# Kernel tuning notes

Hardware: AMD Instinct MI355X
Metric: run time of the kernel (lower is better)

## Reference

```python
import jax, jax.numpy as jnp
import numpy as np

B, S, H, NH, NL = 8, 768, 768, 12, 5
HD = H // NH


def setup_inputs() -> dict:
    key = jax.random.key(0)
    ks = jax.random.split(key, 14)
    lim = 1.0 / np.sqrt(H)
    u = lambda k, shape: jax.random.uniform(k, shape, jnp.float32, -lim, lim)
    inp = {}
    inp["hidden_states"] = jax.random.normal(ks[0], (B, S, H), jnp.float32)
    inp["language_ids"] = jax.random.randint(ks[1], (B,), 0, NL)
    inp["attention_mask"] = jnp.ones((B, S), jnp.int32)
    # per-language query/key Linear weights (torch Linear: y = x @ W.T + b)
    inp["Wq_lang"] = u(ks[2], (NL, H, H))
    inp["bq_lang"] = u(ks[3], (NL, H))
    inp["Wk_lang"] = u(ks[4], (NL, H, H))
    inp["bk_lang"] = u(ks[5], (NL, H))
    # nn.MultiheadAttention params
    inp["in_proj_w"] = u(ks[6], (3 * H, H))
    inp["in_proj_b"] = u(ks[7], (3 * H,))
    inp["out_proj_w"] = u(ks[8], (H, H))
    inp["out_proj_b"] = u(ks[9], (H,))
    # alignment matrices: initialized as eye in torch; perturb so products are non-trivial
    inp["align"] = jnp.eye(H, dtype=jnp.float32) + 0.02 * jax.random.normal(ks[10], (NL, NL, H, H), jnp.float32)
    # output projection + layer norm
    inp["proj_w"] = u(ks[11], (H, H))
    inp["proj_b"] = u(ks[12], (H,))
    inp["ln_g"] = jnp.ones((H,), jnp.float32)
    inp["ln_b"] = jnp.zeros((H,), jnp.float32)
    return inp


def reference(hidden_states, language_ids, attention_mask, Wq_lang, bq_lang, Wk_lang, bk_lang,
              in_proj_w, in_proj_b, out_proj_w, out_proj_b, align, proj_w, proj_b, ln_g, ln_b):
    b, s, h = hidden_states.shape
    lang = language_ids
    # language-routed query/key transforms (grouped GEMM via gather of per-lang weights)
    q = jnp.einsum('bsi,boi->bso', hidden_states, Wq_lang[lang]) + bq_lang[lang][:, None, :]
    k = jnp.einsum('bsi,boi->bso', hidden_states, Wk_lang[lang]) + bk_lang[lang][:, None, :]
    # nn.MultiheadAttention (eval mode, no dropout). Note: the torch module's
    # key_padding_mask is always all-False due to a masked_fill(-inf).bool() bug,
    # so no masking is applied -- reproduced faithfully here.
    wq, wk, wv = jnp.split(in_proj_w, 3, axis=0)
    bq_, bk_, bv_ = jnp.split(in_proj_b, 3)
    Q = (jnp.einsum('bsi,oi->bso', q, wq) + bq_).reshape(b, s, NH, HD)
    K = (jnp.einsum('bsi,oi->bso', k, wk) + bk_).reshape(b, s, NH, HD)
    V = (jnp.einsum('bsi,oi->bso', hidden_states, wv) + bv_).reshape(b, s, NH, HD)
    scores = jnp.einsum('bqhd,bkhd->bhqk', Q, K) / np.sqrt(HD).astype(np.float32)
    attn = jax.nn.softmax(scores, axis=-1)  # [b, nh, s, s]
    ctx = jnp.einsum('bhqk,bkhd->bqhd', attn, V).reshape(b, s, h)
    aligned = jnp.einsum('bsi,oi->bso', ctx, out_proj_w) + out_proj_b
    # pairwise alignment chain: for each i, aligned_i @ prod_{j: lang_j != lang_i} A[lang_i, lang_j]
    # (i==j skipped; same-language pairs skipped since no A exists)
    same = lang[:, None] == lang[None, :]  # [b, b]; diagonal is True -> identity
    sel = align[lang[:, None], lang[None, :]]  # [b, b, h, h]
    I = jnp.eye(h, dtype=hidden_states.dtype)
    Smat = jnp.where(same[:, :, None, None], I, sel)  # [b(i), b(j), h, h]
    def step(carry, Sj):  # carry [b,h,h], Sj [b,h,h] for one j across all i
        return carry @ Sj, None
    M, _ = jax.lax.scan(step, jnp.tile(I, (b, 1, 1)), jnp.swapaxes(Smat, 0, 1))
    aligned = jnp.einsum('bsh,bhk->bsk', aligned, M)
    # output projection + residual layer norm
    out = jnp.einsum('bsi,oi->bso', aligned, proj_w) + proj_b
    x = out + hidden_states
    mu = x.mean(-1, keepdims=True)
    var = x.var(-1, keepdims=True)
    return (x - mu) / jnp.sqrt(var + 1e-5) * ln_g + ln_b
```

## Files before the change

kernel.cpp:

```cpp
#include <hip/hip_runtime.h>

#define Bn 8
#define Sn 768
#define Hn 768
#define NHn 12
#define HDn 64
#define NLn 5

typedef unsigned short u16;
typedef __bf16 bf16x8 __attribute__((ext_vector_type(8)));
typedef short s16x8 __attribute__((ext_vector_type(8)));
typedef float f32x4 __attribute__((ext_vector_type(4)));
typedef unsigned short u16x4 __attribute__((ext_vector_type(4)));

static __device__ __forceinline__ float bf2f(u16 v) {
    return __uint_as_float(((unsigned)v) << 16);
}
static __device__ __forceinline__ u16 f2bf(float f) {
    unsigned u = __float_as_uint(f);
    unsigned r = u + 0x7fffu + ((u >> 16) & 1u);
    return (u16)(r >> 16);
}
static __device__ __forceinline__ bf16x8 ld8(const u16* p) {
    return *reinterpret_cast<const bf16x8*>(p);
}
static __device__ __forceinline__ void glds16(const u16* g, u16* l) {
    __builtin_amdgcn_global_load_lds(
        (const __attribute__((address_space(1))) void*)g,
        (__attribute__((address_space(3))) void*)l, 16, 0, 0);
}

__global__ __launch_bounds__(256) void k_f2b3(
    const float* __restrict__ s0, u16* __restrict__ d0, int n0,
    const float* __restrict__ s1, u16* __restrict__ d1, int n1,
    const float* __restrict__ s2, u16* __restrict__ d2, int n2)
{
    int i = blockIdx.x * 256 + threadIdx.x;
    const float* s; u16* d; int off;
    if (i < n0)                { s = s0; d = d0; off = i; }
    else if (i < n0 + n1)      { s = s1; d = d1; off = i - n0; }
    else if (i < n0 + n1 + n2) { s = s2; d = d2; off = i - n0 - n1; }
    else return;
    float4 v = reinterpret_cast<const float4*>(s)[off];
    u16x4 o;
    o[0] = f2bf(v.x); o[1] = f2bf(v.y); o[2] = f2bf(v.z); o[3] = f2bf(v.w);
    reinterpret_cast<u16x4*>(d)[off] = o;
}

__global__ __launch_bounds__(256) void k_f2b1(
    const float* __restrict__ s, u16* __restrict__ d, int n)
{
    int i = blockIdx.x * 256 + threadIdx.x;
    if (i >= n) return;
    float4 v = reinterpret_cast<const float4*>(s)[i];
    u16x4 o;
    o[0] = f2bf(v.x); o[1] = f2bf(v.y); o[2] = f2bf(v.z); o[3] = f2bf(v.w);
    reinterpret_cast<u16x4*>(d)[i] = o;
}

__global__ __launch_bounds__(256) void k_transpose11(
    const float* __restrict__ Wq, const float* __restrict__ Wk,
    const float* __restrict__ opw, u16* __restrict__ S, u16* __restrict__ opwT)
{
    __shared__ float T[64][65];
    const size_t HH = (size_t)Hn * Hn;
    int z = blockIdx.z;
    const float* src;
    u16* dst;
    if (z < 5)       { src = Wq + (size_t)z * HH;       dst = S + (size_t)z * HH; }
    else if (z < 10) { src = Wk + (size_t)(z - 5) * HH; dst = S + (size_t)z * HH; }
    else             { src = opw;                        dst = opwT; }
    int i0 = blockIdx.x * 64, o0 = blockIdx.y * 64;
    int x = threadIdx.x & 63, ys = threadIdx.x >> 6;
    for (int r = ys; r < 64; r += 4)
        T[r][x] = src[(size_t)(o0 + r) * Hn + i0 + x];
    __syncthreads();
    for (int r = ys; r < 64; r += 4)
        dst[(size_t)(i0 + r) * Hn + o0 + x] = f2bf(T[x][r]);
}

__device__ __forceinline__ void gemm128(
    const u16* __restrict__ A, int lda,
    const u16* __restrict__ Bw, int ldb,
    const float* __restrict__ bias,
    const float* __restrict__ addres,
    u16* __restrict__ outH, float* __restrict__ outF,
    u16* __restrict__ outVT, int ldc,
    int K, int m0, int n0, float scale)
{
    __shared__ u16 As[2][128 * 32];
    __shared__ u16 Bs[2][128 * 32];
    const int tid = threadIdx.x;
    const int lane = tid & 63, wave = tid >> 6;
    const int lrow = lane & 15, lquad = lane >> 4;
    const int wm = (wave >> 1) * 64, wn = (wave & 1) * 64;

    const int s0 = tid, s1 = tid + 256;
    const u16* gA0 = A + (size_t)(m0 + (s0 >> 2)) * lda + (s0 & 3) * 8;
    const u16* gA1 = A + (size_t)(m0 + (s1 >> 2)) * lda + (s1 & 3) * 8;
    const u16* gB0 = Bw + (size_t)(n0 + (s0 >> 2)) * ldb + (s0 & 3) * 8;
    const u16* gB1 = Bw + (size_t)(n0 + (s1 >> 2)) * ldb + (s1 & 3) * 8;

    f32x4 z = {0.f, 0.f, 0.f, 0.f};
    f32x4 acc[4][4];
    #pragma unroll
    for (int i = 0; i < 4; ++i)
        #pragma unroll
        for (int j = 0; j < 4; ++j) acc[i][j] = z;

    const int NT = K >> 5;
    auto stage = [&](int buf, int k0) {
        glds16(gA0 + k0, &As[buf][s0 * 8]);
        glds16(gA1 + k0, &As[buf][s1 * 8]);
        glds16(gB0 + k0, &Bs[buf][s0 * 8]);
        glds16(gB1 + k0, &Bs[buf][s1 * 8]);
    };
    auto compute = [&](int buf) {
        bf16x8 af[4], bf_[4];
        #pragma unroll
        for (int i = 0; i < 4; ++i)
            af[i] = ld8(&As[buf][(wm + i * 16 + lrow) * 32 + lquad * 8]);
        #pragma unroll
        for (int j = 0; j < 4; ++j)
            bf_[j] = ld8(&Bs[buf][(wn + j * 16 + lrow) * 32 + lquad * 8]);
        #pragma unroll
        for (int i = 0; i < 4; ++i)
            #pragma unroll
            for (int j = 0; j < 4; ++j)
                acc[i][j] = __builtin_amdgcn_mfma_f32_16x16x32_bf16(af[i], bf_[j], acc[i][j], 0, 0, 0);
    };

    stage(0, 0);
    __syncthreads();
    for (int kt = 1; kt < NT; ++kt) {
        stage(kt & 1, kt * 32);
        compute((kt - 1) & 1);
        __syncthreads();
    }
    compute((NT - 1) & 1);

    #pragma unroll
    for (int i = 0; i < 4; ++i) {
        #pragma unroll
        for (int j = 0; j < 4; ++j) {
            int col = n0 + wn + j * 16 + lrow;
            float bv = bias ? bias[col] : 0.f;
            if (outVT) {
                int row0 = m0 + wm + i * 16 + lquad * 4;
                int bb = row0 / Sn, s = row0 % Sn;
                int hh = col >> 6, dd = col & 63;
                u16x4 o;
                #pragma unroll
                for (int r = 0; r < 4; ++r) o[r] = f2bf((acc[i][j][r] + bv) * scale);
                *reinterpret_cast<u16x4*>(
                    outVT + (((size_t)bb * NHn + hh) * 64 + dd) * Sn + s) = o;
            } else {
                #pragma unroll
                for (int r = 0; r < 4; ++r) {
                    int row = m0 + wm + i * 16 + lquad * 4 + r;
                    float v = (acc[i][j][r] + bv) * scale;
                    if (addres) v += addres[(size_t)row * ldc + col];
                    if (outF) outF[(size_t)row * ldc + col] = v;
                    else      outH[(size_t)row * ldc + col] = f2bf(v);
                }
            }
        }
    }
}

__device__ __forceinline__ void gemm64(
    const u16* __restrict__ A, const u16* __restrict__ Bw,
    u16* __restrict__ outH, int K, int m0, int n0)
{
    __shared__ u16 As[2][64 * 32];
    __shared__ u16 Bs[2][64 * 32];
    const int tid = threadIdx.x;
    const int lane = tid & 63, wave = tid >> 6;
    const int lrow = lane & 15, lquad = lane >> 4;
    const int wm = (wave >> 1) * 32, wn = (wave & 1) * 32;

    const int row = tid >> 2, seg = tid & 3;
    const u16* gA = A + (size_t)(m0 + row) * Hn + seg * 8;
    const u16* gB = Bw + (size_t)(n0 + row) * Hn + seg * 8;

    f32x4 z = {0.f, 0.f, 0.f, 0.f};
    f32x4 acc[2][2];
    #pragma unroll
    for (int i = 0; i < 2; ++i)
        #pragma unroll
        for (int j = 0; j < 2; ++j) acc[i][j] = z;

    const int NT = K >> 5;
    auto stage = [&](int buf, int k0) {
        glds16(gA + k0, &As[buf][tid * 8]);
        glds16(gB + k0, &Bs[buf][tid * 8]);
    };
    auto compute = [&](int buf) {
        bf16x8 af[2], bf_[2];
        #pragma unroll
        for (int i = 0; i < 2; ++i)
            af[i] = ld8(&As[buf][(wm + i * 16 + lrow) * 32 + lquad * 8]);
        #pragma unroll
        for (int j = 0; j < 2; ++j)
            bf_[j] = ld8(&Bs[buf][(wn + j * 16 + lrow) * 32 + lquad * 8]);
        #pragma unroll
        for (int i = 0; i < 2; ++i)
            #pragma unroll
            for (int j = 0; j < 2; ++j)
                acc[i][j] = __builtin_amdgcn_mfma_f32_16x16x32_bf16(af[i], bf_[j], acc[i][j], 0, 0, 0);
    };

    stage(0, 0);
    __syncthreads();
    for (int kt = 1; kt < NT; ++kt) {
        stage(kt & 1, kt * 32);
        compute((kt - 1) & 1);
        __syncthreads();
    }
    compute((NT - 1) & 1);

    #pragma unroll
    for (int i = 0; i < 2; ++i)
        #pragma unroll
        for (int j = 0; j < 2; ++j) {
            int col = n0 + wn + j * 16 + lrow;
            #pragma unroll
            for (int r = 0; r < 4; ++r) {
                int row_ = m0 + wm + i * 16 + lquad * 4 + r;
                outH[(size_t)row_ * Hn + col] = f2bf(acc[i][j][r]);
            }
        }
}


__global__ __launch_bounds__(256) void k_gemm_qkv(
    const u16* __restrict__ A,
    const u16* __restrict__ Sq, const u16* __restrict__ Sk,
    const u16* __restrict__ Wv,
    const float* __restrict__ beff, const float* __restrict__ ipb,
    const int* __restrict__ lang,
    u16* __restrict__ outQ, u16* __restrict__ outK, u16* __restrict__ outVT)
{
    const size_t HH = (size_t)Hn * Hn;
    int z = blockIdx.z;
    int m0 = blockIdx.x * 128, n0 = blockIdx.y * 128;
    int l = lang[blockIdx.x / 6];
    if (z == 0) {
        gemm128(A, Hn, Sq + (size_t)l * HH, Hn, beff + (size_t)l * Hn,
                nullptr, outQ, nullptr, nullptr, Hn, Hn, m0, n0, 0.125f);
    } else if (z == 1) {
        gemm128(A, Hn, Sk + (size_t)l * HH, Hn, beff + (size_t)(5 + l) * Hn,
                nullptr, outK, nullptr, nullptr, Hn, Hn, m0, n0, 1.f);
    } else {
        gemm128(A, Hn, Wv, Hn, ipb + 2 * Hn,
                nullptr, nullptr, nullptr, outVT, Hn, Hn, m0, n0, 1.f);
    }
}

__global__ __launch_bounds__(256) void k_gemm_act(
    const u16* __restrict__ A, const u16* __restrict__ W5,
    const float* __restrict__ bias5, const int* __restrict__ lang,
    u16* __restrict__ out, float scale)
{
    int b = blockIdx.x / 6;
    int l = lang ? lang[b] : 0;
    gemm128(A, Hn, W5 + (size_t)l * Hn * Hn, Hn,
            bias5 + (size_t)l * Hn, nullptr, out, nullptr, nullptr, Hn, Hn,
            blockIdx.x * 128, blockIdx.y * 128, scale);
}

__global__ __launch_bounds__(256) void k_comb10(
    const u16* __restrict__ ipwb, u16* __restrict__ S)
{
    const size_t HH = (size_t)Hn * Hn;
    int z = blockIdx.z;
    const u16* Aop = ipwb + (z < 5 ? 0 : HH);
    gemm128(Aop, Hn, S + (size_t)z * HH, Hn, nullptr, nullptr,
            S + (size_t)(10 + z) * HH, nullptr, nullptr, Hn, Hn,
            blockIdx.x * 128, blockIdx.y * 128, 1.f);
}

__global__ __launch_bounds__(256) void k_ybuild64(
    const u16* __restrict__ MT5, const u16* __restrict__ Bfix,
    u16* __restrict__ out5)
{
    size_t off = (size_t)blockIdx.z * Hn * Hn;
    gemm64(MT5 + off, Bfix, out5 + off, Hn,
           blockIdx.x * 64, blockIdx.y * 64);
}

__global__ __launch_bounds__(256) void k_xgemm(
    const u16* __restrict__ A, const u16* __restrict__ W,
    const float* __restrict__ bias, const float* __restrict__ hidden,
    float* __restrict__ x)
{
    gemm128(A, Hn, W, Hn, bias, hidden, nullptr, x, nullptr, Hn, Hn,
            blockIdx.x * 128, blockIdx.y * 128, 1.f);
}

__global__ __launch_bounds__(256) void k_chain_first(
    const u16* __restrict__ alignb, const int* __restrict__ lang,
    u16* __restrict__ out5)
{
    const size_t HH = (size_t)Hn * Hn;
    int l = blockIdx.z, lj = lang[Bn - 1];
    u16* dst = out5 + (size_t)l * HH;
    int i0 = blockIdx.x * 64, o0 = blockIdx.y * 64;
    const int tid = threadIdx.x;
    if (lj == l) {
        #pragma unroll
        for (int it = 0; it < 2; ++it) {
            int s = tid + 256 * it;
            int ri = s >> 3, c8 = s & 7;
            s16x8 v;
            #pragma unroll
            for (int e = 0; e < 8; ++e)
                v[e] = (short)((i0 + ri == o0 + c8 * 8 + e) ? 0x3F80 : 0);
            *reinterpret_cast<s16x8*>(dst + (size_t)(i0 + ri) * Hn + o0 + c8 * 8) = v;
        }
    } else {
        const u16* src = alignb + ((size_t)l * NLn + lj) * HH;
        __shared__ u16 T[64][72];
        #pragma unroll
        for (int it = 0; it < 2; ++it) {
            int s = tid + 256 * it;
            int r = s >> 3, c8 = s & 7;
            s16x8 v = *reinterpret_cast<const s16x8*>(
                src + (size_t)(o0 + r) * Hn + i0 + c8 * 8);
            #pragma unroll
            for (int e = 0; e < 8; ++e) T[c8 * 8 + e][r] = (u16)v[e];
        }
        __syncthreads();
        #pragma unroll
        for (int it = 0; it < 2; ++it) {
            int s = tid + 256 * it;
            int ri = s >> 3, c8 = s & 7;
            s16x8 v = *reinterpret_cast<const s16x8*>(&T[ri][c8 * 8]);
            *reinterpret_cast<s16x8*>(dst + (size_t)(i0 + ri) * Hn + o0 + c8 * 8) = v;
        }
    }
}

__global__ __launch_bounds__(256) void k_chain64(
    const u16* __restrict__ Pin, u16* __restrict__ Pout,
    const u16* __restrict__ alignb, const int* __restrict__ lang, int j)
{
    const size_t HH = (size_t)Hn * Hn;
    int l = blockIdx.z;
    int lj = lang[j];
    const u16* Pl = Pin + (size_t)l * HH;
    u16* Po = Pout + (size_t)l * HH;
    int m0 = blockIdx.x * 64, n0 = blockIdx.y * 64;
    if (lj == l) {
        int tid = threadIdx.x;
        #pragma unroll
        for (int it = 0; it < 2; ++it) {
            int s = tid + 256 * it;
            int row = s >> 3, seg = s & 7;
            *reinterpret_cast<s16x8*>(Po + (size_t)(m0 + row) * Hn + n0 + seg * 8) =
                *reinterpret_cast<const s16x8*>(Pl + (size_t)(m0 + row) * Hn + n0 + seg * 8);
        }
    } else {
        const u16* F = alignb + ((size_t)l * NLn + lj) * HH;
        gemm64(Pl, F, Po, Hn, m0, n0);
    }
}

__global__ __launch_bounds__(256) void k_biasqk(
    const float* __restrict__ ipw, const float* __restrict__ ipb,
    const float* __restrict__ bq_lang, const float* __restrict__ bk_lang,
    float* __restrict__ beff)
{
    int o = blockIdx.x * 256 + threadIdx.x;
    int which = blockIdx.y / 5, l = blockIdx.y % 5;
    const float4* w = reinterpret_cast<const float4*>(ipw + (size_t)which * Hn * Hn + (size_t)o * Hn);
    const float4* bv = reinterpret_cast<const float4*>(((which ? bk_lang : bq_lang) + (size_t)l * Hn));
    float s = 0.f;
    for (int j = 0; j < Hn / 4; ++j) {
        float4 a = w[j], b = bv[j];
        s += a.x * b.x + a.y * b.y + a.z * b.z + a.w * b.w;
    }
    s += ipb[which * Hn + o];
    beff[(size_t)(which * 5 + l) * Hn + o] = s;
}

__global__ __launch_bounds__(256) void k_opbeff(
    const float* __restrict__ opb, const u16* __restrict__ MT5,
    float* __restrict__ out)
{
    int n = blockIdx.x * 256 + threadIdx.x;
    int l = blockIdx.y;
    const u16* mt = MT5 + ((size_t)l * Hn + n) * Hn;
    float s = 0.f;
    for (int k = 0; k < Hn; k += 8) {
        s16x8 v = *reinterpret_cast<const s16x8*>(mt + k);
        #pragma unroll
        for (int j = 0; j < 8; ++j) s += opb[k + j] * bf2f((u16)v[j]);
    }
    out[(size_t)l * Hn + n] = s;
}

__global__ __launch_bounds__(256) void k_attn(
    const u16* __restrict__ Q, const u16* __restrict__ K,
    const u16* __restrict__ VT, u16* __restrict__ ctx)
{
    __shared__ u16 Ks[2][64 * 64];
    __shared__ u16 Vs[64 * 64];
    __shared__ u16 Pw[4][16 * 72];

    const int bz = blockIdx.z, h = blockIdx.y, q0 = blockIdx.x * 64;
    const int tid = threadIdx.x;
    const int wave = tid >> 6, lane = tid & 63;
    const int lrow = lane & 15, lquad = lane >> 4;
    const int sw = lrow & 7;

    const u16* Qp = Q + ((size_t)(bz * Sn + q0 + wave * 16 + lrow)) * Hn + h * HDn;
    const u16* Kb = K + (size_t)bz * Sn * Hn + h * HDn;
    const u16* Vb = VT + ((size_t)(bz * NHn + h) * 64) * Sn;

    bf16x8 qa0 = ld8(Qp + lquad * 8);
    bf16x8 qa1 = ld8(Qp + 32 + lquad * 8);

    f32x4 z4 = {0.f, 0.f, 0.f, 0.f};
    float m_r[4], l_l[4];
    f32x4 oacc[4];
    #pragma unroll
    for (int r = 0; r < 4; ++r) { m_r[r] = -1e30f; l_l[r] = 0.f; }
    #pragma unroll
    for (int jd = 0; jd < 4; ++jd) oacc[jd] = z4;

    const int vd0 = tid >> 3,        vp0 = (tid & 7) ^ (vd0 & 7);
    const int vd1 = (tid + 256) >> 3, vp1 = ((tid + 256) & 7) ^ (vd1 & 7);
    const u16* vg0 = Vb + (size_t)vd0 * Sn + vp0 * 8;
    const u16* vg1 = Vb + (size_t)vd1 * Sn + vp1 * 8;
    s16x8 vr0, vr1;

    auto vload = [&](int t0) {
        vr0 = *reinterpret_cast<const s16x8*>(vg0 + t0);
        vr1 = *reinterpret_cast<const s16x8*>(vg1 + t0);
    };
    auto vstore = [&]() {
        *reinterpret_cast<s16x8*>(&Vs[tid * 8]) = vr0;
        *reinterpret_cast<s16x8*>(&Vs[(tid + 256) * 8]) = vr1;
    };
    auto stageK = [&](int t0, int buf) {
        #pragma unroll
        for (int it = 0; it < 2; ++it) {
            int idx = tid + 256 * it;
            int row = idx >> 3, p = idx & 7;
            glds16(Kb + (size_t)(t0 + row) * Hn + (p ^ (row & 7)) * 8,
                   &Ks[buf][idx * 8]);
        }
    };

    auto compute = [&](int buf) {
        f32x4 sc[4];
        __builtin_amdgcn_s_setprio(1);
        #pragma unroll
        for (int j = 0; j < 4; ++j) {
            int base = (j * 16 + lrow) * 64 + ((lquad ^ sw) * 8);
            f32x4 s = __builtin_amdgcn_mfma_f32_16x16x32_bf16(qa0, ld8(&Ks[buf][base]), z4, 0, 0, 0);
            sc[j] = __builtin_amdgcn_mfma_f32_16x16x32_bf16(qa1, ld8(&Ks[buf][base ^ 32]), s, 0, 0, 0);
        }
        __builtin_amdgcn_s_setprio(0);
        float tmax[4];
        #pragma unroll
        for (int r = 0; r < 4; ++r)
            tmax[r] = fmaxf(fmaxf(sc[0][r], sc[1][r]), fmaxf(sc[2][r], sc[3][r]));
        #pragma unroll
        for (int off = 1; off < 16; off <<= 1)
            #pragma unroll
            for (int r = 0; r < 4; ++r)
                tmax[r] = fmaxf(tmax[r], __shfl_xor(tmax[r], off));
        bool grow = (tmax[0] > m_r[0]) | (tmax[1] > m_r[1]) |
                    (tmax[2] > m_r[2]) | (tmax[3] > m_r[3]);
        if (grow) {
            #pragma unroll
            for (int r = 0; r < 4; ++r) {
                float mn = fmaxf(m_r[r], tmax[r]);
                float a = __expf(m_r[r] - mn);
                m_r[r] = mn;
                l_l[r] *= a;
                #pragma unroll
                for (int jd = 0; jd < 4; ++jd) oacc[jd][r] *= a;
            }
        }
        float ps[4] = {0.f, 0.f, 0.f, 0.f};
        #pragma unroll
        for (int j = 0; j < 4; ++j)
            #pragma unroll
            for (int r = 0; r < 4; ++r) {
                float p = __expf(sc[j][r] - m_r[r]);
                ps[r] += p;
                Pw[wave][(lquad * 4 + r) * 72 + j * 16 + lrow] = f2bf(p);
            }
        #pragma unroll
        for (int r = 0; r < 4; ++r) l_l[r] += ps[r];
        bf16x8 pa0 = ld8(&Pw[wave][lrow * 72 + lquad * 8]);
        bf16x8 pa1 = ld8(&Pw[wave][lrow * 72 + 32 + lquad * 8]);
        __builtin_amdgcn_s_setprio(1);
        #pragma unroll
        for (int jd = 0; jd < 4; ++jd) {
            int vbase = (jd * 16 + lrow) * 64 + ((lquad ^ sw) * 8);
            oacc[jd] = __builtin_amdgcn_mfma_f32_16x16x32_bf16(pa0, ld8(&Vs[vbase]), oacc[jd], 0, 0, 0);
            oacc[jd] = __builtin_amdgcn_mfma_f32_16x16x32_bf16(pa1, ld8(&Vs[vbase ^ 32]), oacc[jd], 0, 0, 0);
        }
        __builtin_amdgcn_s_setprio(0);
    };

    stageK(0, 0);
    vload(0);
    vstore();
    __syncthreads();
    for (int kt = 0; kt < 12; ++kt) {
        if (kt < 11) {
            vload((kt + 1) * 64);
            stageK((kt + 1) * 64, (kt + 1) & 1);
        }
        compute(kt & 1);
        if (kt < 11) {
            __syncthreads();
            vstore();
            __syncthreads();
        }
    }

    #pragma unroll
    for (int off = 1; off < 16; off <<= 1)
        #pragma unroll
        for (int r = 0; r < 4; ++r)
            l_l[r] += __shfl_xor(l_l[r], off);

    float rl[4];
    #pragma unroll
    for (int r = 0; r < 4; ++r) rl[r] = 1.f / l_l[r];
    #pragma unroll
    for (int jd = 0; jd < 4; ++jd)
        #pragma unroll
        for (int r = 0; r < 4; ++r) {
            size_t row = (size_t)bz * Sn + q0 + wave * 16 + lquad * 4 + r;
            ctx[row * Hn + h * HDn + jd * 16 + lrow] = f2bf(oacc[jd][r] * rl[r]);
        }
}

__global__ __launch_bounds__(64) void k_ln(
    float* x, const float* __restrict__ g, const float* __restrict__ beta)
{
    size_t row = blockIdx.x;
    float* xr = x + row * Hn;
    int lane = threadIdx.x;
    float v[12];
    float s = 0.f, ss = 0.f;
    #pragma unroll
    for (int i = 0; i < 12; ++i) {
        v[i] = xr[lane + i * 64];
        s += v[i];
        ss += v[i] * v[i];
    }
    #pragma unroll
    for (int off = 1; off < 64; off <<= 1) {
        s  += __shfl_xor(s, off);
        ss += __shfl_xor(ss, off);
    }
    float mu = s * (1.f / Hn);
    float var = ss * (1.f / Hn) - mu * mu;
    float inv = rsqrtf(var + 1e-5f);
    #pragma unroll
    for (int i = 0; i < 12; ++i) {
        int c = lane + i * 64;
        xr[c] = (v[i] - mu) * inv * g[c] + beta[c];
    }
}

extern "C" void kernel_launch(void* const* d_in, const int* in_sizes, int n_in,
                              void* d_out, int out_size, void* d_ws, size_t ws_size,
                              hipStream_t stream)
{
    (void)in_sizes; (void)n_in; (void)out_size; (void)ws_size;

    const float* hidden  = (const float*)d_in[0];
    const int*   lang    = (const int*)d_in[1];
    const float* Wq_lang = (const float*)d_in[3];
    const float* bq_lang = (const float*)d_in[4];
    const float* Wk_lang = (const float*)d_in[5];
    const float* bk_lang = (const float*)d_in[6];
    const float* ipw     = (const float*)d_in[7];
    const float* ipb     = (const float*)d_in[8];
    const float* opw     = (const float*)d_in[9];
    const float* opb     = (const float*)d_in[10];
    const float* align   = (const float*)d_in[11];
    const float* projw   = (const float*)d_in[12];
    const float* projb   = (const float*)d_in[13];
    const float* ln_g    = (const float*)d_in[14];
    const float* ln_b    = (const float*)d_in[15];
    float* out = (float*)d_out;

    const size_t HH  = (size_t)Hn * Hn;
    const size_t BSH = (size_t)Bn * Sn * Hn;
    const size_t AHH = (size_t)NLn * NLn * HH;

    u16* rA = (u16*)d_ws;
    u16* rB = rA + BSH;
    u16* rC = rB + BSH;
    u16* rD = rC + BSH;
    u16* ipwb = rD + BSH;
    u16* pjwb = ipwb + 3 * HH;
    u16* opwT = pjwb + HH;
    u16* alignb = opwT + HH;
    float* beff   = (float*)(alignb + AHH);
    float* opbeff = beff + 10 * Hn;

    u16* S = alignb;

    {
        int n0 = (int)(BSH / 4), n1 = (int)(3 * HH / 4), n2 = (int)(HH / 4);
        k_f2b3<<<(unsigned)((n0 + n1 + n2 + 255) / 256), 256, 0, stream>>>(
            hidden, rA, n0, ipw, ipwb, n1, projw, pjwb, n2);
    }
    k_transpose11<<<dim3(12, 12, 11), 256, 0, stream>>>(Wq_lang, Wk_lang, opw, S, opwT);
    k_biasqk<<<dim3(3, 10), 256, 0, stream>>>(ipw, ipb, bq_lang, bk_lang, beff);

    k_comb10<<<dim3(6, 6, 10), 256, 0, stream>>>(ipwb, S);

    k_gemm_qkv<<<dim3(48, 6, 3), 256, 0, stream>>>(
        rA, S + 10 * HH, S + 15 * HH, ipwb + 2 * HH, beff, ipb, lang, rB, rC, rD);

    k_f2b1<<<(unsigned)(AHH / 4 / 256), 256, 0, stream>>>(align, alignb, (int)(AHH / 4));

    k_attn<<<dim3(12, NHn, Bn), 256, 0, stream>>>(rB, rC, rD, rA);

    k_chain_first<<<dim3(12, 12, NLn), 256, 0, stream>>>(alignb, lang, rC);
    u16* Pin = rC;
    u16* Pout = rD;
    for (int j = Bn - 2; j >= 0; --j) {
        k_chain64<<<dim3(12, 12, NLn), 256, 0, stream>>>(Pin, Pout, alignb, lang, j);
        u16* t = Pin; Pin = Pout; Pout = t;
    }

    k_opbeff<<<dim3(3, NLn), 256, 0, stream>>>(opb, Pin, opbeff);
    k_ybuild64<<<dim3(12, 12, NLn), 256, 0, stream>>>(Pin, opwT, Pout);

    k_gemm_act<<<dim3(48, 6), 256, 0, stream>>>(rA, Pout, opbeff, lang, rB, 1.f);
    k_xgemm<<<dim3(48, 6), 256, 0, stream>>>(rB, pjwb, projb, hidden, out);
    k_ln<<<(unsigned)(Bn * Sn), 64, 0, stream>>>(out, ln_g, ln_b);
}
```

Measured before the change: 543.8 us.

## Fold output projection into per-language weights, merge prep kernels, widen attention blocks

Merges the conversion, transpose and bias-precompute kernels into one launch. Pre-multiplies the projection weight, the alignment chain product and the out-projection weight into one per-language 768x768 matrix with a combined bias, so the activation path needs a single GEMM instead of two. This removes a full B*S*H activation GEMM at the cost of extra weight-sized GEMMs (5x two 768^3). Attention blocks now use 512 threads and 128 queries each, which halves the grid and doubles the K/V reuse per staged tile. The folded product may also change bf16 rounding.

```diff
diff --git a/kernel.cpp b/kernel.cpp
--- a/kernel.cpp
+++ b/kernel.cpp
@@ -30,21 +30,64 @@
         (__attribute__((address_space(3))) void*)l, 16, 0, 0);
 }
 
-__global__ __launch_bounds__(256) void k_f2b3(
-    const float* __restrict__ s0, u16* __restrict__ d0, int n0,
-    const float* __restrict__ s1, u16* __restrict__ d1, int n1,
-    const float* __restrict__ s2, u16* __restrict__ d2, int n2)
-{
-    int i = blockIdx.x * 256 + threadIdx.x;
-    const float* s; u16* d; int off;
-    if (i < n0)                { s = s0; d = d0; off = i; }
-    else if (i < n0 + n1)      { s = s1; d = d1; off = i - n0; }
-    else if (i < n0 + n1 + n2) { s = s2; d = d2; off = i - n0 - n1; }
-    else return;
-    float4 v = reinterpret_cast<const float4*>(s)[off];
-    u16x4 o;
-    o[0] = f2bf(v.x); o[1] = f2bf(v.y); o[2] = f2bf(v.z); o[3] = f2bf(v.w);
-    reinterpret_cast<u16x4*>(d)[off] = o;
+#define PREP_NF2B 6912
+#define PREP_NTR  1584
+__global__ __launch_bounds__(256) void k_prep(
+    const float* __restrict__ hidden, u16* __restrict__ hb,
+    const float* __restrict__ ipw, u16* __restrict__ ipwb,
+    const float* __restrict__ projw, u16* __restrict__ pjwb,
+    const float* __restrict__ Wq, const float* __restrict__ Wk,
+    const float* __restrict__ opw, u16* __restrict__ S, u16* __restrict__ opwT,
+    const float* __restrict__ ipb,
+    const float* __restrict__ bq_lang, const float* __restrict__ bk_lang,
+    float* __restrict__ beff)
+{
+    __shared__ float T[64][65];
+    const size_t HH = (size_t)Hn * Hn;
+    const int bid = blockIdx.x, tid = threadIdx.x;
+    if (bid < PREP_NF2B) {
+        const int n0 = (int)(Bn * Sn * Hn / 4), n1 = (int)(3 * HH / 4), n2 = (int)(HH / 4);
+        int i = bid * 256 + tid;
+        const float* s; u16* d; int off;
+        if (i < n0)                { s = hidden; d = hb;   off = i; }
+        else if (i < n0 + n1)      { s = ipw;    d = ipwb; off = i - n0; }
+        else if (i < n0 + n1 + n2) { s = projw;  d = pjwb; off = i - n0 - n1; }
+        else return;
+        float4 v = reinterpret_cast<const float4*>(s)[off];
+        u16x4 o;
+        o[0] = f2bf(v.x); o[1] = f2bf(v.y); o[2] = f2bf(v.z); o[3] = f2bf(v.w);
+        reinterpret_cast<u16x4*>(d)[off] = o;
+    } else if (bid < PREP_NF2B + PREP_NTR) {
+        int b2 = bid - PREP_NF2B;
+        int z = b2 / 144, r = b2 % 144;
+        int bx = r % 12, by = r / 12;
+        const float* src;
+        u16* dst;
+        if (z < 5)       { src = Wq + (size_t)z * HH;       dst = S + (size_t)z * HH; }
+        else if (z < 10) { src = Wk + (size_t)(z - 5) * HH; dst = S + (size_t)z * HH; }
+        else             { src = opw;                        dst = opwT; }
+        int i0 = bx * 64, o0 = by * 64;
+        int x = tid & 63, ys = tid >> 6;
+        for (int rr = ys; rr < 64; rr += 4)
+            T[rr][x] = src[(size_t)(o0 + rr) * Hn + i0 + x];
+        __syncthreads();
+        for (int rr = ys; rr < 64; rr += 4)
+            dst[(size_t)(i0 + rr) * Hn + o0 + x] = f2bf(T[x][rr]);
+    } else {
+        int b3 = bid - PREP_NF2B - PREP_NTR;
+        int ox = b3 % 3, y = b3 / 3;
+        int o = ox * 256 + tid;
+        int which = y / 5, l = y % 5;
+        const float4* w = reinterpret_cast<const float4*>(ipw + (size_t)which * HH + (size_t)o * Hn);
+        const float4* bv = reinterpret_cast<const float4*>(((which ? bk_lang : bq_lang) + (size_t)l * Hn));
+        float s = 0.f;
+        for (int j = 0; j < Hn / 4; ++j) {
+            float4 a = w[j], b = bv[j];
+            s += a.x * b.x + a.y * b.y + a.z * b.z + a.w * b.w;
+        }
+        s += ipb[which * Hn + o];
+        beff[(size_t)(which * 5 + l) * Hn + o] = s;
+    }
 }
 
 __global__ __launch_bounds__(256) void k_f2b1(
@@ -56,27 +99,6 @@
     u16x4 o;
     o[0] = f2bf(v.x); o[1] = f2bf(v.y); o[2] = f2bf(v.z); o[3] = f2bf(v.w);
     reinterpret_cast<u16x4*>(d)[i] = o;
-}
-
-__global__ __launch_bounds__(256) void k_transpose11(
-    const float* __restrict__ Wq, const float* __restrict__ Wk,
-    const float* __restrict__ opw, u16* __restrict__ S, u16* __restrict__ opwT)
-{
-    __shared__ float T[64][65];
-    const size_t HH = (size_t)Hn * Hn;
-    int z = blockIdx.z;
-    const float* src;
-    u16* dst;
-    if (z < 5)       { src = Wq + (size_t)z * HH;       dst = S + (size_t)z * HH; }
-    else if (z < 10) { src = Wk + (size_t)(z - 5) * HH; dst = S + (size_t)z * HH; }
-    else             { src = opw;                        dst = opwT; }
-    int i0 = blockIdx.x * 64, o0 = blockIdx.y * 64;
-    int x = threadIdx.x & 63, ys = threadIdx.x >> 6;
-    for (int r = ys; r < 64; r += 4)
-        T[r][x] = src[(size_t)(o0 + r) * Hn + i0 + x];
-    __syncthreads();
-    for (int r = ys; r < 64; r += 4)
-        dst[(size_t)(i0 + r) * Hn + o0 + x] = f2bf(T[x][r]);
 }
 
 __device__ __forceinline__ void gemm128(
@@ -257,18 +279,6 @@
     }
 }
 
-__global__ __launch_bounds__(256) void k_gemm_act(
-    const u16* __restrict__ A, const u16* __restrict__ W5,
-    const float* __restrict__ bias5, const int* __restrict__ lang,
-    u16* __restrict__ out, float scale)
-{
-    int b = blockIdx.x / 6;
-    int l = lang ? lang[b] : 0;
-    gemm128(A, Hn, W5 + (size_t)l * Hn * Hn, Hn,
-            bias5 + (size_t)l * Hn, nullptr, out, nullptr, nullptr, Hn, Hn,
-            blockIdx.x * 128, blockIdx.y * 128, scale);
-}
-
 __global__ __launch_bounds__(256) void k_comb10(
     const u16* __restrict__ ipwb, u16* __restrict__ S)
 {
@@ -277,24 +287,6 @@
     const u16* Aop = ipwb + (z < 5 ? 0 : HH);
     gemm128(Aop, Hn, S + (size_t)z * HH, Hn, nullptr, nullptr,
             S + (size_t)(10 + z) * HH, nullptr, nullptr, Hn, Hn,
-            blockIdx.x * 128, blockIdx.y * 128, 1.f);
-}
-
-__global__ __launch_bounds__(256) void k_ybuild64(
-    const u16* __restrict__ MT5, const u16* __restrict__ Bfix,
-    u16* __restrict__ out5)
-{
-    size_t off = (size_t)blockIdx.z * Hn * Hn;
-    gemm64(MT5 + off, Bfix, out5 + off, Hn,
-           blockIdx.x * 64, blockIdx.y * 64);
-}
-
-__global__ __launch_bounds__(256) void k_xgemm(
-    const u16* __restrict__ A, const u16* __restrict__ W,
-    const float* __restrict__ bias, const float* __restrict__ hidden,
-    float* __restrict__ x)
-{
-    gemm128(A, Hn, W, Hn, bias, hidden, nullptr, x, nullptr, Hn, Hn,
             blockIdx.x * 128, blockIdx.y * 128, 1.f);
 }
 
@@ -366,49 +358,79 @@
     }
 }
 
-__global__ __launch_bounds__(256) void k_biasqk(
-    const float* __restrict__ ipw, const float* __restrict__ ipb,
-    const float* __restrict__ bq_lang, const float* __restrict__ bk_lang,
-    float* __restrict__ beff)
-{
-    int o = blockIdx.x * 256 + threadIdx.x;
-    int which = blockIdx.y / 5, l = blockIdx.y % 5;
-    const float4* w = reinterpret_cast<const float4*>(ipw + (size_t)which * Hn * Hn + (size_t)o * Hn);
-    const float4* bv = reinterpret_cast<const float4*>(((which ? bk_lang : bq_lang) + (size_t)l * Hn));
-    float s = 0.f;
-    for (int j = 0; j < Hn / 4; ++j) {
-        float4 a = w[j], b = bv[j];
-        s += a.x * b.x + a.y * b.y + a.z * b.z + a.w * b.w;
-    }
-    s += ipb[which * Hn + o];
-    beff[(size_t)(which * 5 + l) * Hn + o] = s;
-}
-
-__global__ __launch_bounds__(256) void k_opbeff(
-    const float* __restrict__ opb, const u16* __restrict__ MT5,
-    float* __restrict__ out)
-{
-    int n = blockIdx.x * 256 + threadIdx.x;
-    int l = blockIdx.y;
-    const u16* mt = MT5 + ((size_t)l * Hn + n) * Hn;
-    float s = 0.f;
-    for (int k = 0; k < Hn; k += 8) {
-        s16x8 v = *reinterpret_cast<const s16x8*>(mt + k);
-        #pragma unroll
-        for (int j = 0; j < 8; ++j) s += opb[k + j] * bf2f((u16)v[j]);
-    }
-    out[(size_t)l * Hn + n] = s;
-}
-
-__global__ __launch_bounds__(256) void k_attn(
+__global__ __launch_bounds__(256) void k_uop(
+    const u16* __restrict__ opwT, const u16* __restrict__ MT5,
+    const float* __restrict__ opb,
+    u16* __restrict__ U5, float* __restrict__ opbeff)
+{
+    const size_t HH = (size_t)Hn * Hn;
+    int bid = blockIdx.x;
+    if (bid < 720) {
+        int z = bid / 144, r = bid % 144;
+        gemm64(opwT, MT5 + (size_t)z * HH, U5 + (size_t)z * HH, Hn,
+               (r % 12) * 64, (r / 12) * 64);
+    } else {
+        int b2 = bid - 720;
+        int n = (b2 % 3) * 256 + threadIdx.x;
+        int l = b2 / 3;
+        const u16* mt = MT5 + ((size_t)l * Hn + n) * Hn;
+        float s = 0.f;
+        for (int k = 0; k < Hn; k += 8) {
+            s16x8 v = *reinterpret_cast<const s16x8*>(mt + k);
+            #pragma unroll
+            for (int j = 0; j < 8; ++j) s += opb[k + j] * bf2f((u16)v[j]);
+        }
+        opbeff[(size_t)l * Hn + n] = s;
+    }
+}
+
+__global__ __launch_bounds__(256) void k_wb2(
+    const u16* __restrict__ pjwb, const u16* __restrict__ U5,
+    const float* __restrict__ opbeff, const float* __restrict__ projw,
+    const float* __restrict__ projb,
+    u16* __restrict__ W5, float* __restrict__ bias2)
+{
+    const size_t HH = (size_t)Hn * Hn;
+    int bid = blockIdx.x;
+    if (bid < 720) {
+        int z = bid / 144, r = bid % 144;
+        gemm64(pjwb, U5 + (size_t)z * HH, W5 + (size_t)z * HH, Hn,
+               (r % 12) * 64, (r / 12) * 64);
+    } else {
+        int b2 = bid - 720;
+        int m = (b2 % 3) * 256 + threadIdx.x;
+        int l = b2 / 3;
+        const float4* w = reinterpret_cast<const float4*>(projw + (size_t)m * Hn);
+        const float4* ob = reinterpret_cast<const float4*>(opbeff + (size_t)l * Hn);
+        float s = 0.f;
+        for (int j = 0; j < Hn / 4; ++j) {
+            float4 a = w[j], b = ob[j];
+            s += a.x * b.x + a.y * b.y + a.z * b.z + a.w * b.w;
+        }
+        bias2[(size_t)l * Hn + m] = s + projb[m];
+    }
+}
+
+__global__ __launch_bounds__(256) void k_xfused(
+    const u16* __restrict__ ctx, const u16* __restrict__ W5,
+    const float* __restrict__ bias2, const int* __restrict__ lang,
+    const float* __restrict__ hidden, float* __restrict__ x)
+{
+    int l = lang[blockIdx.x / 6];
+    gemm128(ctx, Hn, W5 + (size_t)l * Hn * Hn, Hn, bias2 + (size_t)l * Hn,
+            hidden, nullptr, x, nullptr, Hn, Hn,
+            blockIdx.x * 128, blockIdx.y * 128, 1.f);
+}
+
+__global__ __launch_bounds__(512) void k_attn(
     const u16* __restrict__ Q, const u16* __restrict__ K,
     const u16* __restrict__ VT, u16* __restrict__ ctx)
 {
     __shared__ u16 Ks[2][64 * 64];
     __shared__ u16 Vs[64 * 64];
-    __shared__ u16 Pw[4][16 * 72];
-
-    const int bz = blockIdx.z, h = blockIdx.y, q0 = blockIdx.x * 64;
+    __shared__ u16 Pw[8][16 * 72];
+
+    const int bz = blockIdx.z, h = blockIdx.y, q0 = blockIdx.x * 128;
     const int tid = threadIdx.x;
     const int wave = tid >> 6, lane = tid & 63;
     const int lrow = lane & 15, lquad = lane >> 4;
@@ -429,28 +451,20 @@
     #pragma unroll
     for (int jd = 0; jd < 4; ++jd) oacc[jd] = z4;
 
-    const int vd0 = tid >> 3,        vp0 = (tid & 7) ^ (vd0 & 7);
-    const int vd1 = (tid + 256) >> 3, vp1 = ((tid + 256) & 7) ^ (vd1 & 7);
+    const int vd0 = tid >> 3, vp0 = (tid & 7) ^ (vd0 & 7);
     const u16* vg0 = Vb + (size_t)vd0 * Sn + vp0 * 8;
-    const u16* vg1 = Vb + (size_t)vd1 * Sn + vp1 * 8;
-    s16x8 vr0, vr1;
+    s16x8 vr0;
 
     auto vload = [&](int t0) {
         vr0 = *reinterpret_cast<const s16x8*>(vg0 + t0);
-        vr1 = *reinterpret_cast<const s16x8*>(vg1 + t0);
     };
     auto vstore = [&]() {
         *reinterpret_cast<s16x8*>(&Vs[tid * 8]) = vr0;
-        *reinterpret_cast<s16x8*>(&Vs[(tid + 256) * 8]) = vr1;
     };
     auto stageK = [&](int t0, int buf) {
-        #pragma unroll
-        for (int it = 0; it < 2; ++it) {
-            int idx = tid + 256 * it;
-            int row = idx >> 3, p = idx & 7;
-            glds16(Kb + (size_t)(t0 + row) * Hn + (p ^ (row & 7)) * 8,
-                   &Ks[buf][idx * 8]);
-        }
+        int row = tid >> 3, p = tid & 7;
+        glds16(Kb + (size_t)(t0 + row) * Hn + (p ^ (row & 7)) * 8,
+               &Ks[buf][tid * 8]);
     };
 
     auto compute = [&](int buf) {
@@ -609,16 +623,14 @@
     u16* alignb = opwT + HH;
     float* beff   = (float*)(alignb + AHH);
     float* opbeff = beff + 10 * Hn;
+    float* bias2  = opbeff + 5 * Hn;
 
     u16* S = alignb;
 
-    {
-        int n0 = (int)(BSH / 4), n1 = (int)(3 * HH / 4), n2 = (int)(HH / 4);
-        k_f2b3<<<(unsigned)((n0 + n1 + n2 + 255) / 256), 256, 0, stream>>>(
-            hidden, rA, n0, ipw, ipwb, n1, projw, pjwb, n2);
-    }
-    k_transpose11<<<dim3(12, 12, 11), 256, 0, stream>>>(Wq_lang, Wk_lang, opw, S, opwT);
-    k_biasqk<<<dim3(3, 10), 256, 0, stream>>>(ipw, ipb, bq_lang, bk_lang, beff);
+    k_prep<<<(unsigned)(PREP_NF2B + PREP_NTR + 30), 256, 0, stream>>>(
+        hidden, rA, ipw, ipwb, projw, pjwb,
+        Wq_lang, Wk_lang, opw, S, opwT,
+        ipb, bq_lang, bk_lang, beff);
 
     k_comb10<<<dim3(6, 6, 10), 256, 0, stream>>>(ipwb, S);
 
@@ -627,7 +639,7 @@
 
     k_f2b1<<<(unsigned)(AHH / 4 / 256), 256, 0, stream>>>(align, alignb, (int)(AHH / 4));
 
-    k_attn<<<dim3(12, NHn, Bn), 256, 0, stream>>>(rB, rC, rD, rA);
+    k_attn<<<dim3(6, NHn, Bn), 512, 0, stream>>>(rB, rC, rD, rA);
 
     k_chain_first<<<dim3(12, 12, NLn), 256, 0, stream>>>(alignb, lang, rC);
     u16* Pin = rC;
@@ -637,10 +649,9 @@
         u16* t = Pin; Pin = Pout; Pout = t;
     }
 
-    k_opbeff<<<dim3(3, NLn), 256, 0, stream>>>(opb, Pin, opbeff);
-    k_ybuild64<<<dim3(12, 12, NLn), 256, 0, stream>>>(Pin, opwT, Pout);
-
-    k_gemm_act<<<dim3(48, 6), 256, 0, stream>>>(rA, Pout, opbeff, lang, rB, 1.f);
-    k_xgemm<<<dim3(48, 6), 256, 0, stream>>>(rB, pjwb, projb, hidden, out);
+    k_uop<<<735, 256, 0, stream>>>(opwT, Pin, opb, rB, opbeff);
+    k_wb2<<<735, 256, 0, stream>>>(pjwb, rB, opbeff, projw, projb, rC, bias2);
+
+    k_xfused<<<dim3(48, 6), 256, 0, stream>>>(rA, rC, bias2, lang, hidden, out);
     k_ln<<<(unsigned)(Bn * Sn), 64, 0, stream>>>(out, ln_g, ln_b);
 }
```

Measured after the change: 538.2 us. Within noise of the previous version (-1.0%).
